# Kernel tuning notes

Measured on AMD Instinct MI355X. Metric: run time of the kernel, lower is better.

## Reference

```python
import jax, jax.numpy as jnp
import numpy as np

D_MODEL = 768
D_STATE = 64
D_CONV = 4
D_INNER = 1536          # expand * d_model
HEADDIM = 64
NHEADS = D_INNER // HEADDIM  # 24
RANK = 8
SCALE = 16.0 / RANK     # lora alpha / rank = 2.0
D_IN_PROJ = 2 * D_INNER + 2 * D_STATE + NHEADS  # 3224
CONV_DIM = D_INNER + 2 * D_STATE                # 1664
EPS = 1e-6


def _rmsnorm(x, w):
    return x * jax.lax.rsqrt(jnp.mean(x * x, axis=-1, keepdims=True) + EPS) * w


def _loop_rope(x, loop_index):
    # per-loop-index RoPE: same rotation applied to every token/position
    inv_freq = 1.0 / (10000.0 ** (jnp.arange(0, D_MODEL, 2, dtype=jnp.float32) / D_MODEL))
    freqs = jnp.float32(loop_index) * inv_freq
    cos_v = jnp.repeat(jnp.cos(freqs), 2)[:D_MODEL].astype(x.dtype)
    sin_v = jnp.repeat(jnp.sin(freqs), 2)[:D_MODEL].astype(x.dtype)
    rot = jnp.stack([-x[..., 1::2], x[..., ::2]], axis=-1).reshape(x.shape)
    return x * cos_v + rot * sin_v


def _mamba2_core(x, in_base, lora_A_in, lora_B_in, conv_w, conv_b, dt_bias,
                 A_log, D_param, gated_norm_w, out_base, lora_A_out, lora_B_out):
    Bsz, L, _ = x.shape
    # LoRA-adapted input projection
    W_in = in_base + SCALE * (lora_B_in @ lora_A_in)          # (3224, 768)
    zxbcdt = x @ W_in.T                                       # (b, l, 3224)
    z = zxbcdt[..., :D_INNER]                                 # gate branch
    xBC = zxbcdt[..., D_INNER:D_INNER + CONV_DIM]             # conv branch
    dt = jax.nn.softplus(zxbcdt[..., -NHEADS:] + dt_bias)     # (b, l, h)
    # depthwise causal conv1d + silu
    xc = jax.lax.conv_general_dilated(
        xBC.transpose(0, 2, 1), conv_w[:, None, :], (1,), [(D_CONV - 1, 0)],
        dimension_numbers=('NCH', 'OIH', 'NCH'), feature_group_count=CONV_DIM)
    xBC = jax.nn.silu(xc.transpose(0, 2, 1) + conv_b)
    xs = xBC[..., :D_INNER].reshape(Bsz, L, NHEADS, HEADDIM)  # (b, l, h, p)
    Bm = xBC[..., D_INNER:D_INNER + D_STATE]                  # (b, l, n)
    Cm = xBC[..., D_INNER + D_STATE:]                         # (b, l, n)
    A = -jnp.exp(A_log)                                       # (h,)
    dA = jnp.exp(dt * A)                                      # (b, l, h)
    # sequential selective scan (same math as chunked SSD)
    def step(h, inp):
        dA_t, dt_t, B_t, C_t, x_t = inp
        h = dA_t[:, :, None, None] * h + jnp.einsum('bh,bn,bhp->bhpn', dt_t, B_t, x_t)
        y = jnp.einsum('bn,bhpn->bhp', C_t, h)
        return h, y
    tm = lambda a: jnp.moveaxis(a, 1, 0)  # time-major
    h0 = jnp.zeros((Bsz, NHEADS, HEADDIM, D_STATE), x.dtype)
    _, y = jax.lax.scan(step, h0, (tm(dA), tm(dt), tm(Bm), tm(Cm), tm(xs)))
    y = jnp.moveaxis(y, 0, 1) + D_param[None, None, :, None] * xs  # skip term
    y = y.reshape(Bsz, L, D_INNER)
    # gated RMSNorm (RMSNormGated): norm(y * silu(z))
    y = _rmsnorm(y * jax.nn.silu(z), gated_norm_w)
    # LoRA-adapted output projection
    W_out = out_base + SCALE * (lora_B_out @ lora_A_out)      # (768, 1536)
    return y @ W_out.T


def _forward(x, x_prompt, in_base, lora_A_in, lora_B_in, conv_w, conv_b, dt_bias,
             A_log, D_param, gated_norm_w, out_base, lora_A_out, lora_B_out,
             loop_norm_w, lifeline_gate, n_loops):
    for i in range(n_loops):
        h = _loop_rope(_rmsnorm(x, loop_norm_w), i)
        h = _mamba2_core(h, in_base, lora_A_in, lora_B_in, conv_w, conv_b, dt_bias,
                         A_log, D_param, gated_norm_w, out_base, lora_A_out, lora_B_out)
        x = h + lifeline_gate * x_prompt   # lifeline gated residual injection
    return x


def setup_inputs() -> dict:
    key = jax.random.key(0)
    ks = jax.random.split(key, 12)
    f32 = jnp.float32
    rn = lambda k, s, sc=0.02: jax.random.normal(k, s, dtype=f32) * sc
    return {
        'x': jax.random.normal(ks[0], (2, 1024, D_MODEL), f32),
        'x_prompt': jax.random.normal(ks[1], (2, 1024, D_MODEL), f32),
        'in_base': rn(ks[2], (D_IN_PROJ, D_MODEL)),
        'lora_A_in': rn(ks[3], (RANK, D_MODEL), 0.1),
        'lora_B_in': rn(ks[4], (D_IN_PROJ, RANK), 0.01),
        'conv_w': rn(ks[5], (CONV_DIM, D_CONV), 0.1),
        'conv_b': jnp.zeros((CONV_DIM,), f32),
        'dt_bias': rn(ks[6], (NHEADS,), 0.5),
        'A_log': jnp.log(jnp.linspace(1.0, 16.0, NHEADS, dtype=f32)),
        'D_param': jnp.ones((NHEADS,), f32),
        'gated_norm_w': jnp.ones((D_INNER,), f32),
        'out_base': rn(ks[7], (D_MODEL, D_INNER)),
        'lora_A_out': rn(ks[8], (RANK, D_INNER), 0.1),
        'lora_B_out': rn(ks[9], (D_MODEL, RANK), 0.01),
        'loop_norm_w': jnp.ones((D_MODEL,), f32),
        'lifeline_gate': jnp.ones((D_MODEL,), f32),
        'n_loops': 2,
    }


def reference(x, x_prompt, in_base, lora_A_in, lora_B_in, conv_w, conv_b, dt_bias,
              A_log, D_param, gated_norm_w, out_base, lora_A_out, lora_B_out,
              loop_norm_w, lifeline_gate, n_loops):
    return _forward(x, x_prompt, in_base, lora_A_in, lora_B_in, conv_w, conv_b, dt_bias,
                    A_log, D_param, gated_norm_w, out_base, lora_A_out, lora_B_out,
                    loop_norm_w, lifeline_gate, n_loops)
```

## Files before the change

kernel.cpp:

```cpp
#include <hip/hip_runtime.h>
#include <hip/hip_bf16.h>
#include <math.h>

#define D_MODEL 768
#define D_STATE 64
#define D_CONV 4
#define D_INNER 1536
#define HEADDIM 64
#define NHEADS 24
#define RANK 8
#define D_IN_PROJ 3224
#define NPAD 3328
#define ZSTR 3328
#define CONV_DIM 1664
#define BSZ 2
#define SEQ 1024
#define NROWS (BSZ*SEQ)
#define SCALE_LORA 2.0f
#define LC 64
#define NCHUNK (SEQ/LC)
#define LSTR 72

typedef __attribute__((ext_vector_type(8))) short bf16x8;
typedef __attribute__((ext_vector_type(4))) float f32x4;


__device__ inline float waveReduceSum(float v) {
#pragma unroll
    for (int m = 32; m; m >>= 1) v += __shfl_xor(v, m, 64);
    return v;
}

template <int NWAVES>
__device__ inline float blockReduceSum(float v) {
    __shared__ float tmp[NWAVES];
    int lane = threadIdx.x & 63, wid = threadIdx.x >> 6;
    v = waveReduceSum(v);
    if (lane == 0) tmp[wid] = v;
    __syncthreads();
    float tot = 0.f;
#pragma unroll
    for (int i = 0; i < NWAVES; i++) tot += tmp[i];
    return tot;
}

__device__ inline float sigmoidf_(float x) { return 1.f / (1.f + expf(-x)); }

__device__ inline unsigned short f2bf(float f) {
    union { float f; unsigned int u; } v; v.f = f;
    unsigned int r = (v.u + 0x7fffu + ((v.u >> 16) & 1u)) >> 16;
    return (unsigned short)r;
}
__device__ inline float bf2f(unsigned short u) {
    union { unsigned int i; float f; } v; v.i = ((unsigned int)u) << 16; return v.f;
}

__device__ inline void load_lds16(const void* g, void* l) {
    __builtin_amdgcn_global_load_lds((const __attribute__((address_space(1))) void*)g,
                                     (__attribute__((address_space(3))) void*)l, 16, 0, 0);
}


__global__ void build_w_in_kernel(const float* __restrict__ base,
                                  const float* __restrict__ lA,
                                  const float* __restrict__ lB,
                                  unsigned short* __restrict__ W) {
    int idx = blockIdx.x * blockDim.x + threadIdx.x;
    if (idx >= NPAD * D_MODEL) return;
    int r = idx / D_MODEL, c = idx - r * D_MODEL;
    if (r >= D_IN_PROJ) { W[idx] = 0; return; }
    float s = 0.f;
#pragma unroll
    for (int k = 0; k < RANK; k++) s += lB[r * RANK + k] * lA[k * D_MODEL + c];
    W[idx] = f2bf(base[(size_t)r * D_MODEL + c] + SCALE_LORA * s);
}

__global__ void build_w_out_kernel(const float* __restrict__ base,
                                   const float* __restrict__ lA,
                                   const float* __restrict__ lB,
                                   unsigned short* __restrict__ W) {
    int idx = blockIdx.x * blockDim.x + threadIdx.x;
    if (idx >= D_MODEL * D_INNER) return;
    int r = idx / D_INNER, c = idx - r * D_INNER;
    float s = 0.f;
#pragma unroll
    for (int k = 0; k < RANK; k++) s += lB[r * RANK + k] * lA[k * D_INNER + c];
    W[idx] = f2bf(base[idx] + SCALE_LORA * s);
}

__global__ __launch_bounds__(384) void rmsrope_kernel(
    const float* __restrict__ x, const float* __restrict__ w,
    unsigned short* __restrict__ out, int loop_i) {
    int row = blockIdx.x;
    const float* xr = x + (size_t)row * D_MODEL;
    int j = threadIdx.x;
    float x0 = xr[2 * j], x1 = xr[2 * j + 1];
    float ss = blockReduceSum<6>(x0 * x0 + x1 * x1);
    float sc = rsqrtf(ss * (1.f / D_MODEL) + 1e-6f);
    float y0 = x0 * sc * w[2 * j];
    float y1 = x1 * sc * w[2 * j + 1];
    float ang = (float)loop_i * expf((float)(2 * j) * (-9.210340371976184f / (float)D_MODEL));
    float c = cosf(ang), sn = sinf(ang);
    unsigned short* orow = out + (size_t)row * D_MODEL;
    orow[2 * j]     = f2bf(y0 * c - y1 * sn);
    orow[2 * j + 1] = f2bf(y1 * c + y0 * sn);
}

template <int MODE>
__global__ __launch_bounds__(256) void gemm_pipe_kernel(
    const unsigned short* __restrict__ A,
    const unsigned short* __restrict__ B,
    void* __restrict__ Cv, int M, int N, int K, int Cstride,
    int Ks, float* __restrict__ dtraw) {
    __shared__ unsigned short lsA[2][128 * 64];
    __shared__ unsigned short lsB[2][128 * 64];
    int t = threadIdx.x;
    int w = t >> 6, lane = t & 63;
    int n0 = blockIdx.x * 128, m0 = blockIdx.y * 128;
    int kbase = blockIdx.z * Ks;
    int wr = w >> 1, wc = w & 1;
    f32x4 acc[4][4];
#pragma unroll
    for (int i = 0; i < 4; i++)
#pragma unroll
        for (int j = 0; j < 4; j++) acc[i][j] = (f32x4){0.f, 0.f, 0.f, 0.f};

#define STAGE(bi, kk0)                                                           \
    {                                                                            \
        _Pragma("unroll")                                                        \
        for (int o = 0; o < 4; o++) {                                            \
            int s = o * 256 + t;                                                 \
            int row = s >> 3, u = s & 7;                                         \
            int usrc = (u ^ (row & 7)) << 3;                                     \
            unsigned short* la = &lsA[bi][(size_t)(o * 256 + (t & ~63)) * 8];    \
            unsigned short* lb = &lsB[bi][(size_t)(o * 256 + (t & ~63)) * 8];    \
            load_lds16(&A[(size_t)(m0 + row) * K + (kk0) + usrc], la);           \
            load_lds16(&B[(size_t)(n0 + row) * K + (kk0) + usrc], lb);           \
        }                                                                        \
    }

    int nk = Ks >> 6;
    STAGE(0, kbase);
    __syncthreads();
    int cur = 0;
    for (int ks = 0; ks < nk; ks++) {
        if (ks + 1 < nk) STAGE(cur ^ 1, kbase + (ks + 1) * 64);
#pragma unroll
        for (int kk = 0; kk < 2; kk++) {
            bf16x8 af[4], bfr[4];
            int u_t = kk * 4 + (lane >> 4);
            int kof = (u_t ^ (lane & 7)) << 3;
#pragma unroll
            for (int i = 0; i < 4; i++) {
                int row = wr * 64 + i * 16 + (lane & 15);
                af[i] = *(const bf16x8*)&lsA[cur][row * 64 + kof];
            }
#pragma unroll
            for (int j = 0; j < 4; j++) {
                int row = wc * 64 + j * 16 + (lane & 15);
                bfr[j] = *(const bf16x8*)&lsB[cur][row * 64 + kof];
            }
#pragma unroll
            for (int i = 0; i < 4; i++)
#pragma unroll
                for (int j = 0; j < 4; j++)
                    acc[i][j] = __builtin_amdgcn_mfma_f32_16x16x32_bf16(af[i], bfr[j], acc[i][j], 0, 0, 0);
        }
        __syncthreads();
        cur ^= 1;
    }
#undef STAGE

#pragma unroll
    for (int i = 0; i < 4; i++) {
#pragma unroll
        for (int j = 0; j < 4; j++) {
#pragma unroll
            for (int r = 0; r < 4; r++) {
                int row = m0 + wr * 64 + i * 16 + (lane >> 4) * 4 + r;
                int col = n0 + wc * 64 + j * 16 + (lane & 15);
                float v = acc[i][j][r];
                if (MODE == 1) {
                    atomicAdd(&((float*)Cv)[(size_t)row * Cstride + col], v);
                } else {
                    ((unsigned short*)Cv)[(size_t)row * Cstride + col] = f2bf(v);
                    if (col >= 3200 && col < 3224) dtraw[row * 24 + (col - 3200)] = v;
                }
            }
        }
    }
}

__global__ void conv_bc_kernel(const unsigned short* __restrict__ zxb,
                               const float* __restrict__ cw,
                               const float* __restrict__ cb, float* __restrict__ xbc) {
    int idx = blockIdx.x * blockDim.x + threadIdx.x;
    if (idx >= NROWS * 128) return;
    int cbc = idx & 127;
    int row = idx >> 7;
    int l = row & (SEQ - 1);
    int ch = 1536 + cbc;
    const unsigned short* base = zxb + (size_t)row * ZSTR + 3072 + cbc;
    float acc = cb[ch];
#pragma unroll
    for (int t = 0; t < 4; t++) {
        int ll = l - 3 + t;
        if (ll >= 0) acc = fmaf(cw[ch * 4 + t], bf2f(base[(size_t)(ll - l) * ZSTR]), acc);
    }
    xbc[idx] = acc * sigmoidf_(acc);
}

__global__ __launch_bounds__(256) void scan_mfma_kernel(
    const unsigned short* __restrict__ zxb,
    const float* __restrict__ xbc,
    const float* __restrict__ dtraw,
    const float* __restrict__ cw, const float* __restrict__ cb,
    const float* __restrict__ dt_bias,
    const float* __restrict__ A_log,
    const float* __restrict__ Dp,
    float* __restrict__ y,
    float* __restrict__ Fbuf,
    float* __restrict__ cumA) {
    __shared__ unsigned short Cc[64][LSTR];
    __shared__ unsigned short Bb[64][LSTR];
    __shared__ unsigned short Xt[64][LSTR];
    __shared__ unsigned short Bw[64][LSTR];
    __shared__ unsigned short Mm[64][LSTR];
    __shared__ float s_lds[64];
    __shared__ float dt_lds[64];

    int blk = blockIdx.x;
    int c = blk % NCHUNK;
    int bh = blk / NCHUNK;
    int h = bh % NHEADS, b = bh / NHEADS;
    int tid = threadIdx.x;
    int w = tid >> 6, lane = tid & 63;
    const int t0 = c * LC;

    if (w == 0) {
        int t = lane;
        size_t row = (size_t)(b * SEQ + t0 + t);
        float raw = dtraw[row * 24 + h] + dt_bias[h];
        float dt_t = raw > 20.f ? raw : log1pf(expf(raw));
        float s = dt_t * (-expf(A_log[h]));
#pragma unroll
        for (int off = 1; off < 64; off <<= 1) {
            float v = __shfl_up(s, off, 64);
            if (lane >= off) s += v;
        }
        s_lds[t] = s;
        dt_lds[t] = dt_t;
        cumA[(size_t)blk * LC + t] = expf(s);
    }

    float breg[16];
#pragma unroll
    for (int k = 0; k < 16; k++) {
        int idx = k * 256 + tid;
        int r = idx >> 6, ci = idx & 63;
        int l = t0 + r;
        size_t grow = (size_t)(b * SEQ + l);
        int ch = h * 64 + ci;
        float accv = cb[ch];
        const unsigned short* xin = zxb + grow * ZSTR + 1536 + ch;
#pragma unroll
        for (int tap = 0; tap < 4; tap++) {
            int ll = l - 3 + tap;
            if (ll >= 0) accv = fmaf(cw[ch * 4 + tap], bf2f(xin[(size_t)(tap - 3) * ZSTR]), accv);
        }
        float xv = accv * sigmoidf_(accv);
        Xt[ci][r] = f2bf(xv);
        float bv = xbc[grow * 128 + ci];
        float cv = xbc[grow * 128 + 64 + ci];
        Cc[r][ci] = f2bf(cv);
        Bb[r][ci] = f2bf(bv);
        breg[k] = bv;
    }
    __syncthreads();

    float s63 = s_lds[63];
#pragma unroll
    for (int k = 0; k < 16; k++) {
        int idx = k * 256 + tid;
        int r = idx >> 6, ci = idx & 63;
        float wu = expf(s63 - s_lds[r]) * dt_lds[r];
        Bw[ci][r] = f2bf(breg[k] * wu);
    }

    f32x4 accG[4];
#pragma unroll
    for (int j = 0; j < 4; j++) accG[j] = (f32x4){0.f, 0.f, 0.f, 0.f};
#pragma unroll
    for (int kk = 0; kk < 2; kk++) {
        int kof = kk * 32 + (lane >> 4) * 8;
        bf16x8 afr = *(const bf16x8*)&Cc[16 * w + (lane & 15)][kof];
#pragma unroll
        for (int j = 0; j < 4; j++) {
            bf16x8 bfr = *(const bf16x8*)&Bb[16 * j + (lane & 15)][kof];
            accG[j] = __builtin_amdgcn_mfma_f32_16x16x32_bf16(afr, bfr, accG[j], 0, 0, 0);
        }
    }
#pragma unroll
    for (int j = 0; j < 4; j++) {
#pragma unroll
        for (int r = 0; r < 4; r++) {
            int t = 16 * w + (lane >> 4) * 4 + r;
            int u = 16 * j + (lane & 15);
            float v = 0.f;
            if (u <= t) v = accG[j][r] * dt_lds[u] * expf(s_lds[t] - s_lds[u]);
            Mm[t][u] = f2bf(v);
        }
    }
    __syncthreads();

    f32x4 accY[4];
#pragma unroll
    for (int j = 0; j < 4; j++) accY[j] = (f32x4){0.f, 0.f, 0.f, 0.f};
#pragma unroll
    for (int kk = 0; kk < 2; kk++) {
        int kof = kk * 32 + (lane >> 4) * 8;
        bf16x8 afr = *(const bf16x8*)&Mm[16 * w + (lane & 15)][kof];
#pragma unroll
        for (int j = 0; j < 4; j++) {
            bf16x8 bfr = *(const bf16x8*)&Xt[16 * j + (lane & 15)][kof];
            accY[j] = __builtin_amdgcn_mfma_f32_16x16x32_bf16(afr, bfr, accY[j], 0, 0, 0);
        }
    }
    float D_h = Dp[h];
#pragma unroll
    for (int j = 0; j < 4; j++) {
#pragma unroll
        for (int r = 0; r < 4; r++) {
            int t = 16 * w + (lane >> 4) * 4 + r;
            int p = 16 * j + (lane & 15);
            size_t row = (size_t)(b * SEQ + t0 + t);
            float xv = bf2f(Xt[p][t]);
            y[row * D_INNER + h * HEADDIM + p] = accY[j][r] + D_h * xv;
        }
    }

    f32x4 accF[4];
#pragma unroll
    for (int j = 0; j < 4; j++) accF[j] = (f32x4){0.f, 0.f, 0.f, 0.f};
#pragma unroll
    for (int kk = 0; kk < 2; kk++) {
        int kof = kk * 32 + (lane >> 4) * 8;
        bf16x8 afr = *(const bf16x8*)&Bw[16 * w + (lane & 15)][kof];
#pragma unroll
        for (int j = 0; j < 4; j++) {
            bf16x8 bfr = *(const bf16x8*)&Xt[16 * j + (lane & 15)][kof];
            accF[j] = __builtin_amdgcn_mfma_f32_16x16x32_bf16(afr, bfr, accF[j], 0, 0, 0);
        }
    }
#pragma unroll
    for (int j = 0; j < 4; j++) {
#pragma unroll
        for (int r = 0; r < 4; r++) {
            int n = 16 * w + (lane >> 4) * 4 + r;
            int p = 16 * j + (lane & 15);
            Fbuf[(size_t)blk * (HEADDIM * D_STATE) + n * HEADDIM + p] = accF[j][r];
        }
    }
}

__global__ __launch_bounds__(256) void combine_kernel(
    const float* __restrict__ Fbuf, const float* __restrict__ cumA,
    float* __restrict__ Hinit) {
    int bh = blockIdx.x >> 4;
    int np = (blockIdx.x & 15) * 256 + threadIdx.x;
    float H = 0.f;
#pragma unroll
    for (int c = 0; c < NCHUNK; c++) {
        size_t idx = (size_t)(bh * NCHUNK + c) * (HEADDIM * D_STATE) + np;
        float pA = cumA[(size_t)(bh * NCHUNK + c) * LC + (LC - 1)];
        Hinit[idx] = H;
        H = fmaf(pA, H, Fbuf[idx]);
    }
}

__global__ __launch_bounds__(256) void ycorr_kernel(
    const float* __restrict__ xbc, const float* __restrict__ cumA,
    const float* __restrict__ Hinit, float* __restrict__ y) {
    int blk = blockIdx.x;
    int c = blk % NCHUNK;
    int bh = blk / NCHUNK;
    int h = bh % NHEADS, b = bh / NHEADS;
    __shared__ float Cd[LC][D_STATE + 1];
    __shared__ float Hs[D_STATE][HEADDIM + 1];
    int tid = threadIdx.x;
    size_t cbase = (size_t)blk * LC;
    size_t hbase = (size_t)blk * (HEADDIM * D_STATE);
#pragma unroll
    for (int k = 0; k < 16; k++) {
        int idx = tid + k * 256;
        int r = idx >> 6, n = idx & 63;
        size_t row = (size_t)(b * SEQ + c * LC + r);
        Cd[r][n] = xbc[row * 128 + 64 + n] * cumA[cbase + r];
        Hs[r][n] = Hinit[hbase + idx];
    }
    __syncthreads();
    int tx = tid & 15, ty = tid >> 4;
    float acc[4][4] = {};
    for (int n = 0; n < D_STATE; n++) {
        float cv[4], hv[4];
#pragma unroll
        for (int i = 0; i < 4; i++) cv[i] = Cd[ty * 4 + i][n];
#pragma unroll
        for (int j = 0; j < 4; j++) hv[j] = Hs[n][tx * 4 + j];
#pragma unroll
        for (int i = 0; i < 4; i++)
#pragma unroll
            for (int j = 0; j < 4; j++)
                acc[i][j] = fmaf(cv[i], hv[j], acc[i][j]);
    }
#pragma unroll
    for (int i = 0; i < 4; i++) {
        int tt = ty * 4 + i;
        size_t row = (size_t)(b * SEQ + c * LC + tt);
#pragma unroll
        for (int j = 0; j < 4; j++) {
            int p = tx * 4 + j;
            size_t oidx = row * D_INNER + h * HEADDIM + p;
            y[oidx] += acc[i][j];
        }
    }
}

__global__ __launch_bounds__(256) void gatenorm_kernel(
    const float* __restrict__ y, const unsigned short* __restrict__ zxb,
    const float* __restrict__ w, unsigned short* __restrict__ out,
    const float* __restrict__ xp, const float* __restrict__ gate,
    float* __restrict__ outbuf) {
    int row = blockIdx.x;
    const unsigned short* z = zxb + (size_t)row * ZSTR;
    const float* yr = y + (size_t)row * D_INNER;
    float g[6];
    float ss = 0.f;
#pragma unroll
    for (int e = 0; e < 6; e++) {
        int idx = threadIdx.x + e * 256;
        float zv = bf2f(z[idx]);
        float gv = yr[idx] * (zv * sigmoidf_(zv));
        g[e] = gv;
        ss += gv * gv;
    }
    ss = blockReduceSum<4>(ss);
    float sc = rsqrtf(ss * (1.f / D_INNER) + 1e-6f);
#pragma unroll
    for (int e = 0; e < 6; e++) {
        int idx = threadIdx.x + e * 256;
        out[(size_t)row * D_INNER + idx] = f2bf(g[e] * sc * w[idx]);
    }
    if (threadIdx.x < 192) {
        int q = threadIdx.x;
        float4 xv4 = ((const float4*)(xp + (size_t)row * D_MODEL))[q];
        float4 g4 = ((const float4*)gate)[q];
        ((float4*)(outbuf + (size_t)row * D_MODEL))[q] =
            make_float4(g4.x * xv4.x, g4.y * xv4.y, g4.z * xv4.z, g4.w * xv4.w);
    }
}

extern "C" void kernel_launch(void* const* d_in, const int* in_sizes, int n_in,
                              void* d_out, int out_size, void* d_ws, size_t ws_size,
                              hipStream_t stream) {
    const float* x        = (const float*)d_in[0];
    const float* x_prompt = (const float*)d_in[1];
    const float* in_base  = (const float*)d_in[2];
    const float* lA_in    = (const float*)d_in[3];
    const float* lB_in    = (const float*)d_in[4];
    const float* conv_w   = (const float*)d_in[5];
    const float* conv_b   = (const float*)d_in[6];
    const float* dt_bias  = (const float*)d_in[7];
    const float* A_log    = (const float*)d_in[8];
    const float* D_param  = (const float*)d_in[9];
    const float* gnw      = (const float*)d_in[10];
    const float* out_base = (const float*)d_in[11];
    const float* lA_out   = (const float*)d_in[12];
    const float* lB_out   = (const float*)d_in[13];
    const float* loop_nw  = (const float*)d_in[14];
    const float* gate     = (const float*)d_in[15];
    float* out = (float*)d_out;

    float* ws_f = (float*)d_ws;
    float* dtraw = ws_f;
    float* xbc   = dtraw + (size_t)NROWS * 24;
    float* ybuf  = xbc   + (size_t)NROWS * 128;
    float* Fbuf  = ybuf  + (size_t)NROWS * D_INNER;
    float* Hinit = Fbuf  + (size_t)BSZ * NHEADS * NCHUNK * HEADDIM * D_STATE;
    float* cumA  = Hinit + (size_t)BSZ * NHEADS * NCHUNK * HEADDIM * D_STATE;
    unsigned short* zxb   = (unsigned short*)(cumA + (size_t)BSZ * NHEADS * NCHUNK * LC);
    unsigned short* W_in  = zxb   + (size_t)NROWS * ZSTR;
    unsigned short* W_out = W_in  + (size_t)NPAD * D_MODEL;
    unsigned short* hbuf  = W_out + (size_t)D_MODEL * D_INNER;
    unsigned short* ygt   = hbuf  + (size_t)NROWS * D_MODEL;

    build_w_in_kernel<<<(NPAD * D_MODEL + 255) / 256, 256, 0, stream>>>(in_base, lA_in, lB_in, W_in);
    build_w_out_kernel<<<(D_MODEL * D_INNER + 255) / 256, 256, 0, stream>>>(out_base, lA_out, lB_out, W_out);

    for (int i = 0; i < 2; i++) {
        const float* xsrc = (i == 0) ? x : out;
        rmsrope_kernel<<<NROWS, 384, 0, stream>>>(xsrc, loop_nw, hbuf, i);

        dim3 g1(NPAD / 128, NROWS / 128, 1);
        gemm_pipe_kernel<2><<<g1, 256, 0, stream>>>(hbuf, W_in, zxb, NROWS, NPAD, D_MODEL, ZSTR,
                                                    D_MODEL, dtraw);

        conv_bc_kernel<<<(NROWS * 128 + 255) / 256, 256, 0, stream>>>(zxb, conv_w, conv_b, xbc);

        scan_mfma_kernel<<<BSZ * NHEADS * NCHUNK, 256, 0, stream>>>(
            zxb, xbc, dtraw, conv_w, conv_b, dt_bias, A_log, D_param, ybuf, Fbuf, cumA);
        combine_kernel<<<BSZ * NHEADS * 16, 256, 0, stream>>>(Fbuf, cumA, Hinit);
        ycorr_kernel<<<BSZ * NHEADS * NCHUNK, 256, 0, stream>>>(xbc, cumA, Hinit, ybuf);

        gatenorm_kernel<<<NROWS, 256, 0, stream>>>(ybuf, zxb, gnw, ygt, x_prompt, gate, out);

        dim3 g2(D_MODEL / 128, NROWS / 128, 4);
        gemm_pipe_kernel<1><<<g2, 256, 0, stream>>>(ygt, W_out, out, NROWS, D_MODEL, D_INNER, D_MODEL,
                                                    D_INNER / 4, nullptr);
    }
}
```

Measured before the change: 330.1 us.

## Fuse chunk-state combine into ycorr, drop split-K atomics, retile GEMMs

Removes the separate combine kernel and its Hinit buffer: each ycorr block recomputes its initial state by sequentially folding the previous chunks' Fbuf entries, and chunk-0 blocks exit early. The out-projection GEMM drops split-K with atomicAdd and instead uses 64x64 tiles that write the result directly, adding the gate*x_prompt lifeline term in the epilogue rather than in gatenorm. The in-projection GEMM moves to 64x128 tiles to launch more blocks. Trade-offs are redundant Fbuf reads that grow with chunk index in ycorr, and a full-K loop per block in the out-projection.

```diff
diff --git a/kernel.cpp b/kernel.cpp
--- a/kernel.cpp
+++ b/kernel.cpp
@@ -106,64 +106,71 @@
     orow[2 * j + 1] = f2bf(y1 * c + y0 * sn);
 }
 
-template <int MODE>
-__global__ __launch_bounds__(256) void gemm_pipe_kernel(
+template <int BMT, int BNT, int MODE>
+__global__ __launch_bounds__(256) void gemm_tile_kernel(
     const unsigned short* __restrict__ A,
     const unsigned short* __restrict__ B,
     void* __restrict__ Cv, int M, int N, int K, int Cstride,
-    int Ks, float* __restrict__ dtraw) {
-    __shared__ unsigned short lsA[2][128 * 64];
-    __shared__ unsigned short lsB[2][128 * 64];
+    float* __restrict__ dtraw,
+    const float* __restrict__ xp, const float* __restrict__ gate) {
+    constexpr int FM = BMT / 32, FN = BNT / 32;
+    __shared__ unsigned short lsA[2][BMT * 64];
+    __shared__ unsigned short lsB[2][BNT * 64];
     int t = threadIdx.x;
     int w = t >> 6, lane = t & 63;
-    int n0 = blockIdx.x * 128, m0 = blockIdx.y * 128;
-    int kbase = blockIdx.z * Ks;
+    int n0 = blockIdx.x * BNT, m0 = blockIdx.y * BMT;
     int wr = w >> 1, wc = w & 1;
-    f32x4 acc[4][4];
-#pragma unroll
-    for (int i = 0; i < 4; i++)
-#pragma unroll
-        for (int j = 0; j < 4; j++) acc[i][j] = (f32x4){0.f, 0.f, 0.f, 0.f};
-
-#define STAGE(bi, kk0)                                                           \
-    {                                                                            \
-        _Pragma("unroll")                                                        \
-        for (int o = 0; o < 4; o++) {                                            \
-            int s = o * 256 + t;                                                 \
-            int row = s >> 3, u = s & 7;                                         \
-            int usrc = (u ^ (row & 7)) << 3;                                     \
-            unsigned short* la = &lsA[bi][(size_t)(o * 256 + (t & ~63)) * 8];    \
-            unsigned short* lb = &lsB[bi][(size_t)(o * 256 + (t & ~63)) * 8];    \
-            load_lds16(&A[(size_t)(m0 + row) * K + (kk0) + usrc], la);           \
-            load_lds16(&B[(size_t)(n0 + row) * K + (kk0) + usrc], lb);           \
-        }                                                                        \
-    }
-
-    int nk = Ks >> 6;
-    STAGE(0, kbase);
+    f32x4 acc[FM][FN];
+#pragma unroll
+    for (int i = 0; i < FM; i++)
+#pragma unroll
+        for (int j = 0; j < FN; j++) acc[i][j] = (f32x4){0.f, 0.f, 0.f, 0.f};
+
+#define STAGE(bi, kk0)                                                            \
+    {                                                                             \
+        _Pragma("unroll")                                                         \
+        for (int o = 0; o < BMT / 32; o++) {                                      \
+            int s = o * 256 + t;                                                  \
+            int row = s >> 3, u = s & 7;                                          \
+            int usrc = (u ^ (row & 7)) << 3;                                      \
+            load_lds16(&A[(size_t)(m0 + row) * K + (kk0) + usrc],                 \
+                       &lsA[bi][(size_t)(o * 256 + (t & ~63)) * 8]);              \
+        }                                                                         \
+        _Pragma("unroll")                                                         \
+        for (int o = 0; o < BNT / 32; o++) {                                      \
+            int s = o * 256 + t;                                                  \
+            int row = s >> 3, u = s & 7;                                          \
+            int usrc = (u ^ (row & 7)) << 3;                                      \
+            load_lds16(&B[(size_t)(n0 + row) * K + (kk0) + usrc],                 \
+                       &lsB[bi][(size_t)(o * 256 + (t & ~63)) * 8]);              \
+        }                                                                         \
+    }
+
+    int nk = K >> 6;
+    STAGE(0, 0);
     __syncthreads();
     int cur = 0;
     for (int ks = 0; ks < nk; ks++) {
-        if (ks + 1 < nk) STAGE(cur ^ 1, kbase + (ks + 1) * 64);
+        if (ks + 1 < nk) STAGE(cur ^ 1, (ks + 1) * 64);
 #pragma unroll
         for (int kk = 0; kk < 2; kk++) {
-            bf16x8 af[4], bfr[4];
+            bf16x8 af[FM], bfr[FN];
             int u_t = kk * 4 + (lane >> 4);
             int kof = (u_t ^ (lane & 7)) << 3;
 #pragma unroll
-            for (int i = 0; i < 4; i++) {
-                int row = wr * 64 + i * 16 + (lane & 15);
+            for (int i = 0; i < FM; i++) {
+                int row = wr * (BMT / 2) + i * 16 + (lane & 15);
                 af[i] = *(const bf16x8*)&lsA[cur][row * 64 + kof];
             }
 #pragma unroll
-            for (int j = 0; j < 4; j++) {
-                int row = wc * 64 + j * 16 + (lane & 15);
+            for (int j = 0; j < FN; j++) {
+                int row = wc * (BNT / 2) + j * 16 + (lane & 15);
                 bfr[j] = *(const bf16x8*)&lsB[cur][row * 64 + kof];
             }
 #pragma unroll
-            for (int i = 0; i < 4; i++)
-#pragma unroll
-                for (int j = 0; j < 4; j++)
+            for (int i = 0; i < FM; i++)
+#pragma unroll
+                for (int j = 0; j < FN; j++)
                     acc[i][j] = __builtin_amdgcn_mfma_f32_16x16x32_bf16(af[i], bfr[j], acc[i][j], 0, 0, 0);
         }
         __syncthreads();
@@ -172,19 +179,20 @@
 #undef STAGE
 
 #pragma unroll
-    for (int i = 0; i < 4; i++) {
-#pragma unroll
-        for (int j = 0; j < 4; j++) {
+    for (int i = 0; i < FM; i++) {
+#pragma unroll
+        for (int j = 0; j < FN; j++) {
 #pragma unroll
             for (int r = 0; r < 4; r++) {
-                int row = m0 + wr * 64 + i * 16 + (lane >> 4) * 4 + r;
-                int col = n0 + wc * 64 + j * 16 + (lane & 15);
+                int row = m0 + wr * (BMT / 2) + i * 16 + (lane >> 4) * 4 + r;
+                int col = n0 + wc * (BNT / 2) + j * 16 + (lane & 15);
                 float v = acc[i][j][r];
-                if (MODE == 1) {
-                    atomicAdd(&((float*)Cv)[(size_t)row * Cstride + col], v);
-                } else {
+                if (MODE == 2) {
                     ((unsigned short*)Cv)[(size_t)row * Cstride + col] = f2bf(v);
                     if (col >= 3200 && col < 3224) dtraw[row * 24 + (col - 3200)] = v;
+                } else {
+                    ((float*)Cv)[(size_t)row * Cstride + col] =
+                        v + gate[col] * xp[(size_t)row * Cstride + col];
                 }
             }
         }
@@ -363,40 +371,39 @@
     }
 }
 
-__global__ __launch_bounds__(256) void combine_kernel(
-    const float* __restrict__ Fbuf, const float* __restrict__ cumA,
-    float* __restrict__ Hinit) {
-    int bh = blockIdx.x >> 4;
-    int np = (blockIdx.x & 15) * 256 + threadIdx.x;
-    float H = 0.f;
-#pragma unroll
-    for (int c = 0; c < NCHUNK; c++) {
-        size_t idx = (size_t)(bh * NCHUNK + c) * (HEADDIM * D_STATE) + np;
-        float pA = cumA[(size_t)(bh * NCHUNK + c) * LC + (LC - 1)];
-        Hinit[idx] = H;
-        H = fmaf(pA, H, Fbuf[idx]);
-    }
-}
-
 __global__ __launch_bounds__(256) void ycorr_kernel(
     const float* __restrict__ xbc, const float* __restrict__ cumA,
-    const float* __restrict__ Hinit, float* __restrict__ y) {
+    const float* __restrict__ Fbuf, float* __restrict__ y) {
     int blk = blockIdx.x;
     int c = blk % NCHUNK;
+    if (c == 0) return;
     int bh = blk / NCHUNK;
     int h = bh % NHEADS, b = bh / NHEADS;
+    int tid = threadIdx.x;
+
+    float H[16];
+#pragma unroll
+    for (int k = 0; k < 16; k++) H[k] = 0.f;
+    for (int cp = 0; cp < c; cp++) {
+        float pA = cumA[(size_t)(bh * NCHUNK + cp) * LC + (LC - 1)];
+        size_t base = (size_t)(bh * NCHUNK + cp) * (HEADDIM * D_STATE);
+#pragma unroll
+        for (int k = 0; k < 16; k++) {
+            size_t idx = base + tid + k * 256;
+            H[k] = fmaf(pA, H[k], Fbuf[idx]);
+        }
+    }
+
     __shared__ float Cd[LC][D_STATE + 1];
     __shared__ float Hs[D_STATE][HEADDIM + 1];
-    int tid = threadIdx.x;
     size_t cbase = (size_t)blk * LC;
-    size_t hbase = (size_t)blk * (HEADDIM * D_STATE);
 #pragma unroll
     for (int k = 0; k < 16; k++) {
         int idx = tid + k * 256;
         int r = idx >> 6, n = idx & 63;
         size_t row = (size_t)(b * SEQ + c * LC + r);
         Cd[r][n] = xbc[row * 128 + 64 + n] * cumA[cbase + r];
-        Hs[r][n] = Hinit[hbase + idx];
+        Hs[idx >> 6][idx & 63] = H[k];
     }
     __syncthreads();
     int tx = tid & 15, ty = tid >> 4;
@@ -428,9 +435,7 @@
 
 __global__ __launch_bounds__(256) void gatenorm_kernel(
     const float* __restrict__ y, const unsigned short* __restrict__ zxb,
-    const float* __restrict__ w, unsigned short* __restrict__ out,
-    const float* __restrict__ xp, const float* __restrict__ gate,
-    float* __restrict__ outbuf) {
+    const float* __restrict__ w, unsigned short* __restrict__ out) {
     int row = blockIdx.x;
     const unsigned short* z = zxb + (size_t)row * ZSTR;
     const float* yr = y + (size_t)row * D_INNER;
@@ -450,13 +455,6 @@
     for (int e = 0; e < 6; e++) {
         int idx = threadIdx.x + e * 256;
         out[(size_t)row * D_INNER + idx] = f2bf(g[e] * sc * w[idx]);
-    }
-    if (threadIdx.x < 192) {
-        int q = threadIdx.x;
-        float4 xv4 = ((const float4*)(xp + (size_t)row * D_MODEL))[q];
-        float4 g4 = ((const float4*)gate)[q];
-        ((float4*)(outbuf + (size_t)row * D_MODEL))[q] =
-            make_float4(g4.x * xv4.x, g4.y * xv4.y, g4.z * xv4.z, g4.w * xv4.w);
     }
 }
 
@@ -486,8 +484,7 @@
     float* xbc   = dtraw + (size_t)NROWS * 24;
     float* ybuf  = xbc   + (size_t)NROWS * 128;
     float* Fbuf  = ybuf  + (size_t)NROWS * D_INNER;
-    float* Hinit = Fbuf  + (size_t)BSZ * NHEADS * NCHUNK * HEADDIM * D_STATE;
-    float* cumA  = Hinit + (size_t)BSZ * NHEADS * NCHUNK * HEADDIM * D_STATE;
+    float* cumA  = Fbuf  + (size_t)BSZ * NHEADS * NCHUNK * HEADDIM * D_STATE;
     unsigned short* zxb   = (unsigned short*)(cumA + (size_t)BSZ * NHEADS * NCHUNK * LC);
     unsigned short* W_in  = zxb   + (size_t)NROWS * ZSTR;
     unsigned short* W_out = W_in  + (size_t)NPAD * D_MODEL;
@@ -501,21 +498,20 @@
         const float* xsrc = (i == 0) ? x : out;
         rmsrope_kernel<<<NROWS, 384, 0, stream>>>(xsrc, loop_nw, hbuf, i);
 
-        dim3 g1(NPAD / 128, NROWS / 128, 1);
-        gemm_pipe_kernel<2><<<g1, 256, 0, stream>>>(hbuf, W_in, zxb, NROWS, NPAD, D_MODEL, ZSTR,
-                                                    D_MODEL, dtraw);
+        dim3 g1(NPAD / 128, NROWS / 64);
+        gemm_tile_kernel<64, 128, 2><<<g1, 256, 0, stream>>>(
+            hbuf, W_in, zxb, NROWS, NPAD, D_MODEL, ZSTR, dtraw, nullptr, nullptr);
 
         conv_bc_kernel<<<(NROWS * 128 + 255) / 256, 256, 0, stream>>>(zxb, conv_w, conv_b, xbc);
 
         scan_mfma_kernel<<<BSZ * NHEADS * NCHUNK, 256, 0, stream>>>(
             zxb, xbc, dtraw, conv_w, conv_b, dt_bias, A_log, D_param, ybuf, Fbuf, cumA);
-        combine_kernel<<<BSZ * NHEADS * 16, 256, 0, stream>>>(Fbuf, cumA, Hinit);
-        ycorr_kernel<<<BSZ * NHEADS * NCHUNK, 256, 0, stream>>>(xbc, cumA, Hinit, ybuf);
-
-        gatenorm_kernel<<<NROWS, 256, 0, stream>>>(ybuf, zxb, gnw, ygt, x_prompt, gate, out);
-
-        dim3 g2(D_MODEL / 128, NROWS / 128, 4);
-        gemm_pipe_kernel<1><<<g2, 256, 0, stream>>>(ygt, W_out, out, NROWS, D_MODEL, D_INNER, D_MODEL,
-                                                    D_INNER / 4, nullptr);
-    }
-}
+        ycorr_kernel<<<BSZ * NHEADS * NCHUNK, 256, 0, stream>>>(xbc, cumA, Fbuf, ybuf);
+
+        gatenorm_kernel<<<NROWS, 256, 0, stream>>>(ybuf, zxb, gnw, ygt);
+
+        dim3 g2(D_MODEL / 64, NROWS / 64);
+        gemm_tile_kernel<64, 64, 3><<<g2, 256, 0, stream>>>(
+            ygt, W_out, out, NROWS, D_MODEL, D_INNER, D_MODEL, nullptr, x_prompt, gate);
+    }
+}
```

Result: no change. 330.0 us (-0.0%).
